# Optimization experiments

Hardware: AMD Instinct MI355X
Metric: run time of the kernel (lower is better)

Reference implementation:

```python
import jax, jax.numpy as jnp
import numpy as np

N_FILT = 80
FILT_DIM = 251
FS = 16000.0
MIN_FREQ = 50.0


def _kernel_gauss(amp, f1, f2, t):
    # Gaussian-windowed (Gabor-like) bandpass impulse response: band edges f1<f2 (Hz)
    fc = 0.5 * (f1 + f2)
    bw = f2 - f1
    return amp * jnp.exp(-2.0 * (jnp.pi * bw) ** 2 * t ** 2) * jnp.cos(2.0 * jnp.pi * fc * t)


def _norm_pm1(ir):
    # per-filter: scale to [-1,1] then zero-mean, matching the torch code
    mn = jnp.min(ir, axis=-1, keepdims=True)
    mx = jnp.max(ir, axis=-1, keepdims=True)
    ir = 2.0 * (ir - mn) / (mx - mn + 1e-6) - 1.0
    return ir - jnp.mean(ir, axis=-1, keepdims=True)


def _build_filters(norm_f1, norm_f2, norm_f3, norm_f4, amp1, amp2):
    N = FILT_DIM
    t = (jnp.arange(1, N + 1, dtype=jnp.float32) / FS)  # linspace(1,N,N)/fs
    mf = MIN_FREQ / FS
    f1 = jnp.clip(jnp.abs(norm_f1) + mf, 0.0, 0.5)
    f2 = jnp.clip(f1 + jnp.abs(norm_f2 - f1) + mf, 0.0, 0.5)
    f3 = jnp.clip(jnp.abs(norm_f3) + mf, 0.0, 0.5)
    f4 = jnp.clip(f3 + jnp.abs(norm_f4 - f3) + mf, 0.0, 0.5)
    a1 = jnp.abs(amp1)[:, None]
    a2 = jnp.abs(amp2)[:, None]
    ir1 = _norm_pm1(_kernel_gauss(a1, (f1 * FS)[:, None], (f2 * FS)[:, None], t[None, :]))
    ir2 = _norm_pm1(_kernel_gauss(a2, (f3 * FS)[:, None], (f4 * FS)[:, None], t[None, :]))
    pad = N // 2
    # cross-correlation of ir1 with ir2 (torch conv1d semantics), padding N//2 -> length N (N odd)
    def xcorr(a, b):
        return jnp.correlate(jnp.pad(a, (pad, pad)), b[::-1], mode='valid')[::-1] if False else jnp.convolve(jnp.pad(a, (pad, pad)), b[::-1], mode='valid')
    casc = jax.vmap(xcorr)(ir1, ir2)  # [N_filt, N]
    casc = _norm_pm1(casc)
    n = jnp.linspace(0.0, N, N)
    window = (0.54 - 0.46 * jnp.cos(2.0 * jnp.pi * n / N)).astype(jnp.float32)
    return casc * window[None, :]  # [N_filt, N]


def setup_inputs() -> dict:
    key = jax.random.key(0)
    ks = jax.random.split(key, 5)
    x = jax.random.normal(ks[0], (8, 1, 64000), dtype=jnp.float32)
    norm_f1 = jax.random.uniform(ks[1], (N_FILT,), dtype=jnp.float32) * 0.3
    norm_f2 = norm_f1 + jax.random.uniform(ks[2], (N_FILT,), dtype=jnp.float32) * 0.05
    norm_f3 = jax.random.uniform(ks[3], (N_FILT,), dtype=jnp.float32) * 0.3
    norm_f4 = norm_f3 + jax.random.uniform(ks[4], (N_FILT,), dtype=jnp.float32) * 0.05
    amp1 = jnp.ones((N_FILT,), dtype=jnp.float32)
    amp2 = jnp.ones((N_FILT,), dtype=jnp.float32)
    return {"x": x, "norm_f1": norm_f1, "norm_f2": norm_f2, "norm_f3": norm_f3,
            "norm_f4": norm_f4, "amp1": amp1, "amp2": amp2}


def reference(x, norm_f1, norm_f2, norm_f3, norm_f4, amp1, amp2):
    filters = _build_filters(norm_f1, norm_f2, norm_f3, norm_f4, amp1, amp2)
    w = filters[:, None, :]  # [O=N_filt, I=1, K]
    out = jax.lax.conv_general_dilated(
        x, w, window_strides=(1,), padding='VALID',
        dimension_numbers=('NCH', 'OIH', 'NCH'))
    return out  # [B, N_filt, T-K+1]
```

## Files before the change

kernel.cpp:

```cpp
#include <hip/hip_runtime.h>

#define FDIM   251
#define NFILT  80
#define KPAD   256
#define T_IN   64000
#define T_OUT  63750
#define NCHUNK 1024
#define XS1OFF 656
#define XSTOT  1300

typedef short bf16x8 __attribute__((ext_vector_type(8)));
typedef float f32x4  __attribute__((ext_vector_type(4)));

__device__ __forceinline__ unsigned short f2bf(float f) {
  unsigned int u = __float_as_uint(f);
  unsigned int r = (u + 0x7fffu + ((u >> 16) & 1u)) >> 16;
  return (unsigned short)r;
}
__device__ __forceinline__ unsigned int packbf(float a, float b) {
  return (unsigned int)f2bf(a) | ((unsigned int)f2bf(b) << 16);
}

__device__ __forceinline__ void norm_pm1_shared(float* a, float* scratch, int tid) {
  float v  = (tid < FDIM) ? a[tid] : 0.f;
  float mn = (tid < FDIM) ? v : 1e30f;
  float mx = (tid < FDIM) ? v : -1e30f;
  #pragma unroll
  for (int o = 32; o > 0; o >>= 1) {
    mn = fminf(mn, __shfl_down(mn, o));
    mx = fmaxf(mx, __shfl_down(mx, o));
  }
  const int wid = tid >> 6;
  if ((tid & 63) == 0) { scratch[wid] = mn; scratch[4 + wid] = mx; }
  __syncthreads();
  if (tid == 0) {
    scratch[0] = fminf(fminf(scratch[0], scratch[1]), fminf(scratch[2], scratch[3]));
    scratch[4] = fmaxf(fmaxf(scratch[4], scratch[5]), fmaxf(scratch[6], scratch[7]));
  }
  __syncthreads();
  const float gmn = scratch[0], gmx = scratch[4];
  const float nv = 2.f * (v - gmn) / (gmx - gmn + 1e-6f) - 1.f;
  __syncthreads();
  float s = (tid < FDIM) ? nv : 0.f;
  #pragma unroll
  for (int o = 32; o > 0; o >>= 1) s += __shfl_down(s, o);
  if ((tid & 63) == 0) scratch[wid] = s;
  __syncthreads();
  if (tid == 0) scratch[0] = (scratch[0] + scratch[1] + scratch[2] + scratch[3]) / 251.f;
  __syncthreads();
  const float mean = scratch[0];
  if (tid < FDIM) a[tid] = nv - mean;
  __syncthreads();
}

__global__ __launch_bounds__(256) void build_filters_kernel(
    const float* __restrict__ nf1, const float* __restrict__ nf2,
    const float* __restrict__ nf3, const float* __restrict__ nf4,
    const float* __restrict__ amp1, const float* __restrict__ amp2,
    unsigned short* __restrict__ Wbf) {
  __shared__ float ir1[FDIM], ir2[FDIM], casc[FDIM];
  __shared__ float scratch[8];
  const int f = blockIdx.x, tid = threadIdx.x;
  const float FS  = 16000.f;
  const float MF  = 50.f / 16000.f;
  const float PIF = 3.14159265358979323846f;
  const float TPI = 6.28318530717958647692f;

  const float f1 = fminf(fmaxf(fabsf(nf1[f]) + MF, 0.f), 0.5f);
  const float f2 = fminf(fmaxf(f1 + fabsf(nf2[f] - f1) + MF, 0.f), 0.5f);
  const float f3 = fminf(fmaxf(fabsf(nf3[f]) + MF, 0.f), 0.5f);
  const float f4 = fminf(fmaxf(f3 + fabsf(nf4[f] - f3) + MF, 0.f), 0.5f);
  const float a1 = fabsf(amp1[f]);
  const float a2 = fabsf(amp2[f]);

  if (tid < FDIM) {
    const float t = (float)(tid + 1) / FS;
    {
      const float fcs = 0.5f * (f1 + f2) * FS, bws = (f2 - f1) * FS;
      const float pb = PIF * bws;
      ir1[tid] = a1 * expf(-2.f * pb * pb * (t * t)) * cosf(TPI * fcs * t);
    }
    {
      const float fcs = 0.5f * (f3 + f4) * FS, bws = (f4 - f3) * FS;
      const float pb = PIF * bws;
      ir2[tid] = a2 * expf(-2.f * pb * pb * (t * t)) * cosf(TPI * fcs * t);
    }
  }
  __syncthreads();
  norm_pm1_shared(ir1, scratch, tid);
  norm_pm1_shared(ir2, scratch, tid);

  if (tid < FDIM) {
    const int i = tid;
    const int plo = (i - 125 > 0) ? (i - 125) : 0;
    const int phi = (i + 125 < 250) ? (i + 125) : 250;
    float s = 0.f;
    for (int p = plo; p <= phi; ++p) s += ir1[p] * ir2[p + 125 - i];
    casc[i] = s;
  }
  __syncthreads();
  norm_pm1_shared(casc, scratch, tid);

  if (tid < KPAD) {
    float v = 0.f;
    if (tid < FDIM) {
      const float win = 0.54f - 0.46f * cosf(TPI * ((float)tid / 250.f));
      v = casc[tid] * win;
    }
    Wbf[(size_t)f * KPAD + tid] = f2bf(v);
  }
}

__global__ __launch_bounds__(256, 2) void conv_mfma_kernel(
    const float* __restrict__ xin, const unsigned short* __restrict__ Wbf,
    float* __restrict__ outp) {
  __shared__ unsigned int xs[XSTOT];
  const int tid = threadIdx.x;
  const int n0  = blockIdx.x * NCHUNK;
  const int b   = blockIdx.y;
  const int l   = tid & 63, w = tid >> 6;
  const int m   = l & 15, h = l >> 4;

  const short* Wp = (const short*)Wbf;
  bf16x8 afr[5][8];
  #pragma unroll
  for (int mt = 0; mt < 5; ++mt)
    #pragma unroll
    for (int c = 0; c < 8; ++c)
      afr[mt][c] = *(const bf16x8*)(Wp + (mt * 16 + m) * KPAD + c * 32 + h * 8);

  const float* xg = xin + (size_t)b * T_IN;
  for (int i = tid; i < 644; i += 256) {
    const int g = n0 + 2 * i;
    const float a0 = (g     < T_IN) ? xg[g]     : 0.f;
    const float a1 = (g + 1 < T_IN) ? xg[g + 1] : 0.f;
    const float a2 = (g + 2 < T_IN) ? xg[g + 2] : 0.f;
    xs[i]          = packbf(a0, a1);
    xs[XS1OFF + i] = packbf(a1, a2);
  }
  __syncthreads();

  const unsigned int* psrc = xs + ((m & 1) ? XS1OFF : 0);
  const int lane_off = (8 * h + (m & ~1)) >> 1;

  for (int i = 0; i < 16; ++i) {
    const int t_loc = i * 64 + w * 16;
    const int bbase = (t_loc >> 1) + lane_off;

    f32x4 acc[5];
    #pragma unroll
    for (int mt = 0; mt < 5; ++mt) acc[mt] = (f32x4){0.f, 0.f, 0.f, 0.f};

    #pragma unroll
    for (int c = 0; c < 8; ++c) {
      union { unsigned int u[4]; bf16x8 v; } bf;
      bf.u[0] = psrc[bbase + 16 * c + 0];
      bf.u[1] = psrc[bbase + 16 * c + 1];
      bf.u[2] = psrc[bbase + 16 * c + 2];
      bf.u[3] = psrc[bbase + 16 * c + 3];
      #pragma unroll
      for (int mt = 0; mt < 5; ++mt)
        acc[mt] = __builtin_amdgcn_mfma_f32_16x16x32_bf16(afr[mt][c], bf.v, acc[mt], 0, 0, 0);
    }

    const int tglob = n0 + t_loc + m;
    if (tglob < T_OUT) {
      #pragma unroll
      for (int mt = 0; mt < 5; ++mt)
        #pragma unroll
        for (int r = 0; r < 4; ++r) {
          const int f = mt * 16 + 4 * h + r;
          outp[((size_t)b * NFILT + f) * T_OUT + tglob] = acc[mt][r];
        }
    }
  }
}

extern "C" void kernel_launch(void* const* d_in, const int* in_sizes, int n_in,
                              void* d_out, int out_size, void* d_ws, size_t ws_size,
                              hipStream_t stream) {
  const float* x    = (const float*)d_in[0];
  const float* nf1  = (const float*)d_in[1];
  const float* nf2  = (const float*)d_in[2];
  const float* nf3  = (const float*)d_in[3];
  const float* nf4  = (const float*)d_in[4];
  const float* amp1 = (const float*)d_in[5];
  const float* amp2 = (const float*)d_in[6];
  unsigned short* Wbf = (unsigned short*)d_ws;
  float* out = (float*)d_out;

  build_filters_kernel<<<NFILT, 256, 0, stream>>>(nf1, nf2, nf3, nf4, amp1, amp2, Wbf);

  dim3 grid((T_OUT + NCHUNK - 1) / NCHUNK, 8, 1);
  conv_mfma_kernel<<<grid, 256, 0, stream>>>(x, Wbf, out);
}
```

Measured before the change: 62.73 us.

## Use 8 shifted bf16 input copies for vector LDS loads and vectorized stores

Stages eight shifted bf16-pair copies of the input chunk in LDS so each lane can fetch its 8-element MFMA fragment with a single 16-byte load instead of four 4-byte loads. It also swaps the MFMA operand order so each lane holds four consecutive time outputs for one filter. That allows float2 global stores along time rather than scattered scalar stores across filter rows. The cost is about four times more LDS and a heavier staging loop with ten global reads per thread iteration.

```diff
diff --git a/kernel.cpp b/kernel.cpp
--- a/kernel.cpp
+++ b/kernel.cpp
@@ -6,8 +6,8 @@
 #define T_IN   64000
 #define T_OUT  63750
 #define NCHUNK 1024
-#define XS1OFF 656
-#define XSTOT  1300
+#define CPYLEN 648
+#define XSTOT  (8 * CPYLEN)
 
 typedef short bf16x8 __attribute__((ext_vector_type(8)));
 typedef float f32x4  __attribute__((ext_vector_type(4)));
@@ -114,7 +114,7 @@
 __global__ __launch_bounds__(256, 2) void conv_mfma_kernel(
     const float* __restrict__ xin, const unsigned short* __restrict__ Wbf,
     float* __restrict__ outp) {
-  __shared__ unsigned int xs[XSTOT];
+  __shared__ __align__(16) unsigned int xs[XSTOT];
   const int tid = threadIdx.x;
   const int n0  = blockIdx.x * NCHUNK;
   const int b   = blockIdx.y;
@@ -122,30 +122,33 @@
   const int m   = l & 15, h = l >> 4;
 
   const short* Wp = (const short*)Wbf;
-  bf16x8 afr[5][8];
+  bf16x8 wfr[5][8];
   #pragma unroll
   for (int mt = 0; mt < 5; ++mt)
     #pragma unroll
     for (int c = 0; c < 8; ++c)
-      afr[mt][c] = *(const bf16x8*)(Wp + (mt * 16 + m) * KPAD + c * 32 + h * 8);
+      wfr[mt][c] = *(const bf16x8*)(Wp + (mt * 16 + m) * KPAD + c * 32 + h * 8);
 
   const float* xg = xin + (size_t)b * T_IN;
-  for (int i = tid; i < 644; i += 256) {
-    const int g = n0 + 2 * i;
-    const float a0 = (g     < T_IN) ? xg[g]     : 0.f;
-    const float a1 = (g + 1 < T_IN) ? xg[g + 1] : 0.f;
-    const float a2 = (g + 2 < T_IN) ? xg[g + 2] : 0.f;
-    xs[i]          = packbf(a0, a1);
-    xs[XS1OFF + i] = packbf(a1, a2);
+  for (int i = tid; i < CPYLEN - 4; i += 256) {
+    float e[10];
+    #pragma unroll
+    for (int q = 0; q < 10; ++q) {
+      const int g = n0 + 2 * i + q;
+      e[q] = (g < T_IN) ? xg[g] : 0.f;
+    }
+    #pragma unroll
+    for (int j = 0; j < 8; ++j)
+      xs[j * CPYLEN + i] = packbf(e[j], e[j + 1]);
   }
   __syncthreads();
 
-  const unsigned int* psrc = xs + ((m & 1) ? XS1OFF : 0);
-  const int lane_off = (8 * h + (m & ~1)) >> 1;
+  const unsigned int* psrc = xs + (m & 7) * CPYLEN;
+  const int lane_q = h + (m >> 3);
 
   for (int i = 0; i < 16; ++i) {
     const int t_loc = i * 64 + w * 16;
-    const int bbase = (t_loc >> 1) + lane_off;
+    const int q0 = (t_loc >> 3) + lane_q;
 
     f32x4 acc[5];
     #pragma unroll
@@ -153,25 +156,21 @@
 
     #pragma unroll
     for (int c = 0; c < 8; ++c) {
-      union { unsigned int u[4]; bf16x8 v; } bf;
-      bf.u[0] = psrc[bbase + 16 * c + 0];
-      bf.u[1] = psrc[bbase + 16 * c + 1];
-      bf.u[2] = psrc[bbase + 16 * c + 2];
-      bf.u[3] = psrc[bbase + 16 * c + 3];
+      const bf16x8 xf = *(const bf16x8*)(psrc + 4 * (q0 + 4 * c));
       #pragma unroll
       for (int mt = 0; mt < 5; ++mt)
-        acc[mt] = __builtin_amdgcn_mfma_f32_16x16x32_bf16(afr[mt][c], bf.v, acc[mt], 0, 0, 0);
+        acc[mt] = __builtin_amdgcn_mfma_f32_16x16x32_bf16(xf, wfr[mt][c], acc[mt], 0, 0, 0);
     }
 
-    const int tglob = n0 + t_loc + m;
-    if (tglob < T_OUT) {
-      #pragma unroll
-      for (int mt = 0; mt < 5; ++mt)
-        #pragma unroll
-        for (int r = 0; r < 4; ++r) {
-          const int f = mt * 16 + 4 * h + r;
-          outp[((size_t)b * NFILT + f) * T_OUT + tglob] = acc[mt][r];
-        }
+    const int tg = n0 + t_loc + 4 * h;
+    #pragma unroll
+    for (int mt = 0; mt < 5; ++mt) {
+      const int f = mt * 16 + m;
+      const size_t row = ((size_t)b * NFILT + f) * T_OUT;
+      if (tg < T_OUT)
+        *(float2*)&outp[row + tg] = make_float2(acc[mt][0], acc[mt][1]);
+      if (tg + 2 < T_OUT)
+        *(float2*)&outp[row + tg + 2] = make_float2(acc[mt][2], acc[mt][3]);
     }
   }
 }
```

New measurement: 76.17 us. +21.4%, slower.
